# Kernel optimization log

Hardware: AMD Instinct MI355X
Metric: run time of the kernel (lower is better)

## Reference

```python
import jax, jax.numpy as jnp
import numpy as np

B, DIM_IN, DIM_OUT, K, SPK, T = 16, 256, 256, 5, 128, 8192
PAD = (K // 2, K // 2)  # odd kernel -> symmetric reflect pad


def setup_inputs() -> dict:
    key = jax.random.key(0)
    k1, k2, k3, k4 = jax.random.split(key, 4)
    x = jax.random.normal(k1, (B, DIM_IN, T), dtype=jnp.float32)
    c_trg = jax.random.normal(k2, (B, SPK), dtype=jnp.float32)
    # EqualLinear params (bias_init=1, lr_mul=1; forward uses raw weight, no scale)
    style_w = jax.random.normal(k3, (DIM_IN, SPK), dtype=jnp.float32)
    style_b = jnp.ones((DIM_IN,), dtype=jnp.float32)
    # base conv weight [1, dim_out, dim_in, k]
    weight = jax.random.normal(k4, (1, DIM_OUT, DIM_IN, K), dtype=jnp.float32)
    return {"x": x, "c_trg": c_trg, "style_w": style_w, "style_b": style_b, "weight": weight}


def _modulated_conv(x, c_trg, style_w, style_b, weight):
    # style: [B, dim_in]
    s = c_trg @ style_w.T + style_b
    # modulate: [B, dim_out, dim_in, K]
    w = weight * s[:, None, :, None]
    demod = jax.lax.rsqrt(jnp.sum(w * w, axis=(2, 3)) + 1e-8)  # [B, dim_out]
    w = w * demod[:, :, None, None]
    # reflect pad along time
    x_pad = jnp.pad(x, ((0, 0), (0, 0), PAD), mode="reflect")
    # per-sample conv1d (groups=batch in torch) via vmap
    def conv_one(xi, wi):
        # xi: [dim_in, T+K-1], wi: [dim_out, dim_in, K]
        out = jax.lax.conv_general_dilated(
            xi[None], wi, window_strides=(1,), padding="VALID",
            dimension_numbers=("NCH", "OIH", "NCH"))
        return out[0]  # [dim_out, T]
    out = jax.vmap(conv_one)(x_pad, w)
    return jax.nn.leaky_relu(out, negative_slope=0.2)


def reference(x, c_trg, style_w, style_b, weight):
    out = _modulated_conv(x, c_trg, style_w, style_b, weight)
    return (out, c_trg)
```

## Files before the change

kernel.cpp:

```cpp
#include <hip/hip_runtime.h>


#define B_    16
#define CIN   256
#define COUT  256
#define KW    5
#define SPK   128
#define TT    8192

#define OM    128
#define TN    256
#define BI    32
#define NCH   (CIN / BI)

#define XROWS 264
#define WSLAB (KW * OM * 32)
#define WMOD_BYTES ((size_t)B_ * 2 * NCH * WSLAB * 2)

typedef __attribute__((ext_vector_type(8))) short short8;
typedef __attribute__((ext_vector_type(4))) float f32x4;
typedef unsigned short ushort_t;
typedef unsigned int uint_t;

__device__ __forceinline__ ushort_t f2bf(float f) {
    uint_t u = __float_as_uint(f);
    u += 0x7FFF + ((u >> 16) & 1);
    return (ushort_t)(u >> 16);
}

__global__ __launch_bounds__(256) void prep_kernel(
    const float* __restrict__ c_trg, const float* __restrict__ style_w,
    const float* __restrict__ style_b, const float* __restrict__ weight,
    ushort_t* __restrict__ wmod)
{
    __shared__ float c_sh[SPK];
    __shared__ float s_sh[CIN];
    __shared__ float w_l[8 * 1280];
    __shared__ float dm_sh[8];

    const int og  = blockIdx.x;
    const int b   = blockIdx.y;
    const int tid = threadIdx.x;

    if (tid < SPK) c_sh[tid] = c_trg[b * SPK + tid];
    __syncthreads();
    {
        float acc = style_b[tid];
        const float* wr = style_w + (size_t)tid * SPK;
        #pragma unroll 4
        for (int j = 0; j < SPK; ++j) acc += c_sh[j] * wr[j];
        s_sh[tid] = acc;
    }
    {
        const float* wsrc = weight + (size_t)og * 8 * 1280;
        #pragma unroll
        for (int it = 0; it < 10; ++it)
            *(float4*)&w_l[(it * 256 + tid) * 4] = *(const float4*)&wsrc[(it * 256 + tid) * 4];
    }
    __syncthreads();

    {
        const int oi   = tid >> 5;
        const int part = tid & 31;
        float a = 0.f;
        #pragma unroll 8
        for (int m = 0; m < 40; ++m) {
            int j = part + m * 32;
            float v = w_l[oi * 1280 + j] * s_sh[j / 5];
            a += v * v;
        }
        a += __shfl_xor(a, 16);
        a += __shfl_xor(a, 8);
        a += __shfl_xor(a, 4);
        a += __shfl_xor(a, 2);
        a += __shfl_xor(a, 1);
        if (part == 0) dm_sh[oi] = rsqrtf(a + 1e-8f);
    }
    __syncthreads();

    for (int r = tid; r < 320; r += 256) {
        const int oi  = r / 40;
        const int rem = r - oi * 40;
        const int ch  = rem / 5;
        const int k   = rem - ch * 5;
        const int o   = og * 8 + oi;
        const int ot  = o >> 7;
        const int o_l = o & 127;
        const int swz = (o_l >> 1) & 3;
        const float dmv = dm_sh[oi];
        ushort_t* dst = wmod + ((((size_t)(b * 2 + ot) * NCH + ch) * KW + k) * OM + o_l) * 32;
        #pragma unroll
        for (int g = 0; g < 4; ++g) {
            union { ushort_t us[8]; uint4 v; } pk;
            #pragma unroll
            for (int ii = 0; ii < 8; ++ii) {
                int i_l = g * 8 + ii;
                int i_g = ch * 32 + i_l;
                pk.us[ii] = f2bf(w_l[oi * 1280 + i_g * 5 + k] * s_sh[i_g] * dmv);
            }
            *(uint4*)&dst[(g ^ swz) * 8] = pk.v;
        }
    }
}

__global__ __launch_bounds__(512, 2) void conv_mfma_ws3_kernel(
    const float* __restrict__ x, const ushort_t* __restrict__ wmod,
    float* __restrict__ out)
{
    __shared__ __align__(16) ushort_t w_sh[2][WSLAB];
    __shared__ __align__(16) ushort_t x_sh[XROWS * 32];

    const int b   = blockIdx.z;
    const int ot  = blockIdx.y;
    const int o0  = ot * OM;
    const int t0  = blockIdx.x * TN;
    const int tid = threadIdx.x;

    const int lane  = tid & 63;
    const int wv    = tid >> 6;
    const int wm    = wv >> 2;
    const int wn    = wv & 3;
    const int col16 = lane & 15;
    const int quad  = lane >> 4;

    const int rl = lane;
    const int i4 = wv;

    f32x4 acc[4][4];
    #pragma unroll
    for (int mt = 0; mt < 4; ++mt)
        #pragma unroll
        for (int nt = 0; nt < 4; ++nt)
            acc[mt][nt] = (f32x4){0.f, 0.f, 0.f, 0.f};

    const float* xb = x + (size_t)b * CIN * TT;
    const ushort_t* wslab = wmod + (size_t)(b * 2 + ot) * NCH * WSLAB;

    float xr0[20], xr1[20];

#define STAGE_W(CH, BUF) do {                                                  \
        const ushort_t* ws_ = wslab + (size_t)(CH) * WSLAB;                    \
        _Pragma("unroll")                                                      \
        for (int s_ = 0; s_ < 5; ++s_) {                                       \
            const int off_ = s_ * 4096 + wv * 512;           \
            __builtin_amdgcn_global_load_lds(                                  \
                (const __attribute__((address_space(1))) uint_t*)(ws_ + off_ + lane * 8), \
                (__attribute__((address_space(3))) uint_t*)(&w_sh[BUF][off_]), \
                16, 0, 0);                                                     \
        }                                                                      \
    } while (0)

#define LOAD_X(CH, XR) do {                                                    \
        const float* xp_ = xb + (size_t)((CH) * BI + i4 * 4) * TT;             \
        _Pragma("unroll")                                                      \
        for (int rd_ = 0; rd_ < 5; ++rd_) {                                    \
            int r_ = rd_ * 64 + rl;                                            \
            if (r_ < 260) {                                                    \
                int tg_ = t0 + r_ - 2;                                         \
                tg_ = (tg_ < 0) ? -tg_ : tg_;                                  \
                tg_ = (tg_ > TT - 1) ? (2 * (TT - 1) - tg_) : tg_;             \
                XR[rd_ * 4 + 0] = xp_[tg_];                                    \
                XR[rd_ * 4 + 1] = xp_[TT + tg_];                               \
                XR[rd_ * 4 + 2] = xp_[2 * TT + tg_];                           \
                XR[rd_ * 4 + 3] = xp_[3 * TT + tg_];                           \
            }                                                                  \
        }                                                                      \
    } while (0)

#define PUT_X(XR) do {                                                         \
        _Pragma("unroll")                                                      \
        for (int rd_ = 0; rd_ < 5; ++rd_) {                                    \
            int r_ = rd_ * 64 + rl;                                            \
            if (r_ < 260) {                                                    \
                union { ushort_t us[4]; uint2 u2; } p_;                        \
                p_.us[0] = f2bf(XR[rd_ * 4 + 0]);                              \
                p_.us[1] = f2bf(XR[rd_ * 4 + 1]);                              \
                p_.us[2] = f2bf(XR[rd_ * 4 + 2]);                              \
                p_.us[3] = f2bf(XR[rd_ * 4 + 3]);                              \
                int grp_ = (i4 >> 1) ^ ((r_ ^ (r_ >> 2)) & 3);                 \
                *(uint2*)&x_sh[r_ * 32 + grp_ * 8 + (i4 & 1) * 4] = p_.u2;     \
            }                                                                  \
        }                                                                      \
    } while (0)

#define MFMA_CHUNK(BUF) do {                                                   \
        _Pragma("unroll")                                                      \
        for (int kt_ = 0; kt_ < KW; ++kt_) {                                   \
            short8 a_[4], bf_[4];                                              \
            _Pragma("unroll")                                                  \
            for (int mt_ = 0; mt_ < 4; ++mt_) {                                \
                const int row_  = kt_ * OM + wm * 64 + mt_ * 16 + col16;       \
                const int slot_ = quad ^ ((row_ >> 1) & 3);                    \
                a_[mt_] = *(const short8*)&w_sh[BUF][row_ * 32 + slot_ * 8];   \
            }                                                                  \
            _Pragma("unroll")                                                  \
            for (int nt_ = 0; nt_ < 4; ++nt_) {                                \
                const int r_   = wn * 64 + nt_ * 16 + col16 + kt_;             \
                const int grp_ = quad ^ ((r_ ^ (r_ >> 2)) & 3);                \
                bf_[nt_] = *(const short8*)&x_sh[r_ * 32 + grp_ * 8];          \
            }                                                                  \
            _Pragma("unroll")                                                  \
            for (int mt_ = 0; mt_ < 4; ++mt_)                                  \
                _Pragma("unroll")                                              \
                for (int nt_ = 0; nt_ < 4; ++nt_)                              \
                    acc[mt_][nt_] = __builtin_amdgcn_mfma_f32_16x16x32_bf16(   \
                        a_[mt_], bf_[nt_], acc[mt_][nt_], 0, 0, 0);            \
        }                                                                      \
    } while (0)

#define CHUNK_BODY(CH, CUR, NXT, XR_CUR, XR_NXT) do {                          \
        PUT_X(XR_CUR);                                                         \
        __syncthreads();           \
        if ((CH) < NCH - 1) {                                                  \
            STAGE_W((CH) + 1, NXT);                                            \
            LOAD_X((CH) + 1, XR_NXT);                                          \
        }                                                                      \
        __builtin_amdgcn_sched_barrier(0);      \
        MFMA_CHUNK(CUR);                                                       \
        if ((CH) < NCH - 1)                                                    \
            __syncthreads();      \
                                                      \
    } while (0)

    STAGE_W(0, 0);
    LOAD_X(0, xr0);

    CHUNK_BODY(0, 0, 1, xr0, xr1);
    CHUNK_BODY(1, 1, 0, xr1, xr0);
    CHUNK_BODY(2, 0, 1, xr0, xr1);
    CHUNK_BODY(3, 1, 0, xr1, xr0);
    CHUNK_BODY(4, 0, 1, xr0, xr1);
    CHUNK_BODY(5, 1, 0, xr1, xr0);
    CHUNK_BODY(6, 0, 1, xr0, xr1);
    CHUNK_BODY(7, 1, 0, xr1, xr0);

#undef STAGE_W
#undef LOAD_X
#undef PUT_X
#undef MFMA_CHUNK
#undef CHUNK_BODY

    #pragma unroll
    for (int mt = 0; mt < 4; ++mt) {
        #pragma unroll
        for (int nt = 0; nt < 4; ++nt) {
            const int t_o = t0 + wn * 64 + nt * 16 + col16;
            #pragma unroll
            for (int reg = 0; reg < 4; ++reg) {
                const int o_l = wm * 64 + mt * 16 + quad * 4 + reg;
                float v = acc[mt][nt][reg];
                v = (v > 0.f) ? v : 0.2f * v;
                out[((size_t)(b * COUT + o0 + o_l)) * TT + t_o] = v;
            }
        }
    }
}

__global__ __launch_bounds__(256, 3) void conv_mfma_fb_kernel(
    const float* __restrict__ x, const float* __restrict__ c_trg,
    const float* __restrict__ style_w, const float* __restrict__ style_b,
    const float* __restrict__ weight, float* __restrict__ out)
{
    __shared__ ushort_t x_sh[136 * 32];
    __shared__ ushort_t w_sh[KW * 128 * 32];
    __shared__ float    c_sh[SPK];
    __shared__ float    s_sh[CIN];
    __shared__ float    dm_acc[128];
    __shared__ float    dmv[128];

    const int b   = blockIdx.z;
    const int o0  = blockIdx.y * 128;
    const int t0  = blockIdx.x * 128;
    const int tid = threadIdx.x;

    const int lane  = tid & 63;
    const int wvv   = tid >> 6;
    const int wm    = wvv >> 1;
    const int wn    = wvv & 1;
    const int col16 = lane & 15;
    const int quad  = lane >> 4;

    if (tid < SPK) c_sh[tid] = c_trg[b * SPK + tid];
    if (tid < 128) dm_acc[tid] = 0.f;
    __syncthreads();
    {
        float acc = style_b[tid];
        const float* wr = style_w + (size_t)tid * SPK;
        #pragma unroll 4
        for (int j = 0; j < SPK; ++j) acc += c_sh[j] * wr[j];
        s_sh[tid] = acc;
    }

    f32x4 acc[4][4];
    #pragma unroll
    for (int mt = 0; mt < 4; ++mt)
        #pragma unroll
        for (int nt = 0; nt < 4; ++nt)
            acc[mt][nt] = (f32x4){0.f, 0.f, 0.f, 0.f};

    const float* xb = x + (size_t)b * CIN * TT;

    for (int ch = 0; ch < NCH; ++ch) {
        const int i0 = ch * BI;
        __syncthreads();
        {
            const int i4s = tid >> 5;
            const int rls = tid & 31;
            const float* xp = xb + (size_t)(i0 + i4s * 4) * TT;
            #pragma unroll
            for (int rr = 0; rr < 136; rr += 32) {
                int r = rr + rls;
                if (r < 136) {
                    int tg = t0 + r - 2;
                    tg = (tg < 0) ? -tg : tg;
                    tg = (tg > TT - 1) ? (2 * (TT - 1) - tg) : tg;
                    float v0 = xp[tg];
                    float v1 = xp[TT + tg];
                    float v2 = xp[2 * TT + tg];
                    float v3 = xp[3 * TT + tg];
                    union { ushort_t us[4]; uint2 u2; } p;
                    p.us[0] = f2bf(v0); p.us[1] = f2bf(v1);
                    p.us[2] = f2bf(v2); p.us[3] = f2bf(v3);
                    int grp = (i4s >> 1) ^ (r & 3);
                    *(uint2*)&x_sh[r * 32 + grp * 8 + (i4s & 1) * 4] = p.u2;
                }
            }
        }
        {
            const int i4s = tid & 7;
            #pragma unroll
            for (int pass = 0; pass < 4; ++pass) {
                const int o_l = (tid >> 3) + pass * 32;
                const float* wp = weight + ((size_t)(o0 + o_l) * CIN + i0 + i4s * 4) * KW;
                float q[20];
                #pragma unroll
                for (int f = 0; f < 5; ++f)
                    *(float4*)&q[f * 4] = *(const float4*)(wp + f * 4);
                float sv0 = s_sh[i0 + i4s * 4 + 0];
                float sv1 = s_sh[i0 + i4s * 4 + 1];
                float sv2 = s_sh[i0 + i4s * 4 + 2];
                float sv3 = s_sh[i0 + i4s * 4 + 3];
                float m0[5], m1[5], m2[5], m3[5];
                float psum = 0.f;
                #pragma unroll
                for (int k = 0; k < 5; ++k) {
                    m0[k] = q[0 * 5 + k] * sv0;  psum += m0[k] * m0[k];
                    m1[k] = q[1 * 5 + k] * sv1;  psum += m1[k] * m1[k];
                    m2[k] = q[2 * 5 + k] * sv2;  psum += m2[k] * m2[k];
                    m3[k] = q[3 * 5 + k] * sv3;  psum += m3[k] * m3[k];
                }
                atomicAdd(&dm_acc[o_l], psum);
                #pragma unroll
                for (int k = 0; k < 5; ++k) {
                    union { ushort_t us[4]; uint2 u2; } p;
                    p.us[0] = f2bf(m0[k]); p.us[1] = f2bf(m1[k]);
                    p.us[2] = f2bf(m2[k]); p.us[3] = f2bf(m3[k]);
                    *(uint2*)&w_sh[(k * 128 + o_l) * 32 + i4s * 4] = p.u2;
                }
            }
        }
        __syncthreads();
        #pragma unroll
        for (int kt = 0; kt < KW; ++kt) {
            short8 a[4], bf[4];
            #pragma unroll
            for (int mt = 0; mt < 4; ++mt)
                a[mt] = *(const short8*)&w_sh[(kt * 128 + wm * 64 + mt * 16 + col16) * 32 + quad * 8];
            #pragma unroll
            for (int nt = 0; nt < 4; ++nt) {
                int r   = wn * 64 + nt * 16 + col16 + kt;
                int grp = quad ^ (r & 3);
                bf[nt] = *(const short8*)&x_sh[r * 32 + grp * 8];
            }
            #pragma unroll
            for (int mt = 0; mt < 4; ++mt)
                #pragma unroll
                for (int nt = 0; nt < 4; ++nt)
                    acc[mt][nt] = __builtin_amdgcn_mfma_f32_16x16x32_bf16(
                        a[mt], bf[nt], acc[mt][nt], 0, 0, 0);
        }
    }

    __syncthreads();
    if (tid < 128) dmv[tid] = rsqrtf(dm_acc[tid] + 1e-8f);
    __syncthreads();

    #pragma unroll
    for (int mt = 0; mt < 4; ++mt) {
        #pragma unroll
        for (int nt = 0; nt < 4; ++nt) {
            const int t_o = t0 + wn * 64 + nt * 16 + col16;
            #pragma unroll
            for (int reg = 0; reg < 4; ++reg) {
                const int o_l = wm * 64 + mt * 16 + quad * 4 + reg;
                float v = acc[mt][nt][reg] * dmv[o_l];
                v = (v > 0.f) ? v : 0.2f * v;
                out[((size_t)(b * COUT + o0 + o_l)) * TT + t_o] = v;
            }
        }
    }
}

extern "C" void kernel_launch(void* const* d_in, const int* in_sizes, int n_in,
                              void* d_out, int out_size, void* d_ws, size_t ws_size,
                              hipStream_t stream)
{
    const float* x       = (const float*)d_in[0];
    const float* c_trg   = (const float*)d_in[1];
    const float* style_w = (const float*)d_in[2];
    const float* style_b = (const float*)d_in[3];
    const float* weight  = (const float*)d_in[4];
    float* out = (float*)d_out;

    if (ws_size >= WMOD_BYTES) {
        ushort_t* wmod = (ushort_t*)d_ws;
        prep_kernel<<<dim3(32, 16), dim3(256), 0, stream>>>(
            c_trg, style_w, style_b, weight, wmod);
        conv_mfma_ws3_kernel<<<dim3(TT / TN, COUT / OM, B_), dim3(512), 0, stream>>>(
            x, wmod, out);
    } else {
        conv_mfma_fb_kernel<<<dim3(TT / 128, COUT / 128, B_), dim3(256), 0, stream>>>(
            x, c_trg, style_w, style_b, weight, out);
    }

    hipMemcpyAsync(out + (size_t)B_ * COUT * TT, c_trg,
                   (size_t)B_ * SPK * sizeof(float),
                   hipMemcpyDeviceToDevice, stream);
}
```

Before: 307.3 us.

## Apply style scale to input and demod to output instead of per-batch weights

Rather than building a modulated bf16 weight tensor for each batch sample, the prep kernel now converts the base weight to bf16 once, shared across the batch. It also computes the per-sample style vector and the demodulation factors separately. The conv kernel multiplies x by the style scale while converting it to bf16, and multiplies the accumulator by the demod factor in the epilogue. This shrinks the weight workspace by the batch factor, so the weight slabs streamed by the conv kernel are shared across samples and more likely to hit cache. The cost is a small extra multiply per x element and per output. Rounding differs slightly because the style scale is now applied to x before bf16 conversion rather than to the weights.

Result: slower. 336.6 us (+9.5%).

```diff
diff --git a/kernel.cpp b/kernel.cpp
--- a/kernel.cpp
+++ b/kernel.cpp
@@ -15,7 +15,10 @@
 
 #define XROWS 264
 #define WSLAB (KW * OM * 32)
-#define WMOD_BYTES ((size_t)B_ * 2 * NCH * WSLAB * 2)
+#define WBF_BYTES ((size_t)2 * NCH * WSLAB * 2)
+#define S_OFF   WBF_BYTES
+#define DM_OFF  (WBF_BYTES + (size_t)B_ * CIN * 4)
+#define WS_NEED (WBF_BYTES + (size_t)B_ * CIN * 4 * 2)
 
 typedef __attribute__((ext_vector_type(8))) short short8;
 typedef __attribute__((ext_vector_type(4))) float f32x4;
@@ -28,87 +31,91 @@
     return (ushort_t)(u >> 16);
 }
 
-__global__ __launch_bounds__(256) void prep_kernel(
+__global__ __launch_bounds__(256) void prep2_kernel(
     const float* __restrict__ c_trg, const float* __restrict__ style_w,
     const float* __restrict__ style_b, const float* __restrict__ weight,
-    ushort_t* __restrict__ wmod)
+    ushort_t* __restrict__ wbf, float* __restrict__ s_glob,
+    float* __restrict__ dm_glob)
 {
+    __shared__ float sm[8 * 1280];
     __shared__ float c_sh[SPK];
-    __shared__ float s_sh[CIN];
-    __shared__ float w_l[8 * 1280];
-    __shared__ float dm_sh[8];
-
-    const int og  = blockIdx.x;
-    const int b   = blockIdx.y;
+    __shared__ float s2_sh[CIN];
+
     const int tid = threadIdx.x;
 
-    if (tid < SPK) c_sh[tid] = c_trg[b * SPK + tid];
-    __syncthreads();
-    {
+    if (blockIdx.x < 32) {
+        const int og = blockIdx.x;
+        const float* wsrc = weight + (size_t)og * 8 * 1280;
+        #pragma unroll
+        for (int it = 0; it < 10; ++it)
+            *(float4*)&sm[(it * 256 + tid) * 4] = *(const float4*)&wsrc[(it * 256 + tid) * 4];
+        __syncthreads();
+
+        for (int r = tid; r < 320; r += 256) {
+            const int oi  = r / 40;
+            const int rem = r - oi * 40;
+            const int ch  = rem / 5;
+            const int k   = rem - ch * 5;
+            const int o   = og * 8 + oi;
+            const int ot  = o >> 7;
+            const int o_l = o & 127;
+            const int swz = (o_l >> 1) & 3;
+            ushort_t* dst = wbf + (((size_t)(ot * NCH + ch) * KW + k) * OM + o_l) * 32;
+            #pragma unroll
+            for (int g = 0; g < 4; ++g) {
+                union { ushort_t us[8]; uint4 v; } pk;
+                #pragma unroll
+                for (int ii = 0; ii < 8; ++ii) {
+                    int i_g = ch * 32 + g * 8 + ii;
+                    pk.us[ii] = f2bf(sm[oi * 1280 + i_g * 5 + k]);
+                }
+                *(uint4*)&dst[(g ^ swz) * 8] = pk.v;
+            }
+        }
+    } else {
+        const int b = blockIdx.x - 32;
+        if (tid < SPK) c_sh[tid] = c_trg[b * SPK + tid];
+        __syncthreads();
+
         float acc = style_b[tid];
         const float* wr = style_w + (size_t)tid * SPK;
         #pragma unroll 4
         for (int j = 0; j < SPK; ++j) acc += c_sh[j] * wr[j];
-        s_sh[tid] = acc;
-    }
-    {
-        const float* wsrc = weight + (size_t)og * 8 * 1280;
-        #pragma unroll
-        for (int it = 0; it < 10; ++it)
-            *(float4*)&w_l[(it * 256 + tid) * 4] = *(const float4*)&wsrc[(it * 256 + tid) * 4];
-    }
-    __syncthreads();
-
-    {
-        const int oi   = tid >> 5;
-        const int part = tid & 31;
+        s_glob[b * CIN + tid] = acc;
+        s2_sh[tid] = acc * acc;
+        __syncthreads();
+
+        const float* wo = weight + (size_t)tid * 1280;
         float a = 0.f;
-        #pragma unroll 8
-        for (int m = 0; m < 40; ++m) {
-            int j = part + m * 32;
-            float v = w_l[oi * 1280 + j] * s_sh[j / 5];
-            a += v * v;
-        }
-        a += __shfl_xor(a, 16);
-        a += __shfl_xor(a, 8);
-        a += __shfl_xor(a, 4);
-        a += __shfl_xor(a, 2);
-        a += __shfl_xor(a, 1);
-        if (part == 0) dm_sh[oi] = rsqrtf(a + 1e-8f);
-    }
-    __syncthreads();
-
-    for (int r = tid; r < 320; r += 256) {
-        const int oi  = r / 40;
-        const int rem = r - oi * 40;
-        const int ch  = rem / 5;
-        const int k   = rem - ch * 5;
-        const int o   = og * 8 + oi;
-        const int ot  = o >> 7;
-        const int o_l = o & 127;
-        const int swz = (o_l >> 1) & 3;
-        const float dmv = dm_sh[oi];
-        ushort_t* dst = wmod + ((((size_t)(b * 2 + ot) * NCH + ch) * KW + k) * OM + o_l) * 32;
-        #pragma unroll
-        for (int g = 0; g < 4; ++g) {
-            union { ushort_t us[8]; uint4 v; } pk;
-            #pragma unroll
-            for (int ii = 0; ii < 8; ++ii) {
-                int i_l = g * 8 + ii;
-                int i_g = ch * 32 + i_l;
-                pk.us[ii] = f2bf(w_l[oi * 1280 + i_g * 5 + k] * s_sh[i_g] * dmv);
-            }
-            *(uint4*)&dst[(g ^ swz) * 8] = pk.v;
-        }
+        #pragma unroll 4
+        for (int ig = 0; ig < 64; ++ig) {
+            float q[20];
+            #pragma unroll
+            for (int f = 0; f < 5; ++f)
+                *(float4*)&q[f * 4] = *(const float4*)&wo[ig * 20 + f * 4];
+            #pragma unroll
+            for (int c = 0; c < 4; ++c) {
+                const float s2 = s2_sh[ig * 4 + c];
+                #pragma unroll
+                for (int k = 0; k < 5; ++k) {
+                    const float v = q[c * 5 + k];
+                    a += v * v * s2;
+                }
+            }
+        }
+        dm_glob[b * COUT + tid] = rsqrtf(a + 1e-8f);
     }
 }
 
-__global__ __launch_bounds__(512, 2) void conv_mfma_ws3_kernel(
-    const float* __restrict__ x, const ushort_t* __restrict__ wmod,
+__global__ __launch_bounds__(512, 2) void conv_mfma_ws4_kernel(
+    const float* __restrict__ x, const ushort_t* __restrict__ wbf,
+    const float* __restrict__ s_glob, const float* __restrict__ dm_glob,
     float* __restrict__ out)
 {
     __shared__ __align__(16) ushort_t w_sh[2][WSLAB];
     __shared__ __align__(16) ushort_t x_sh[XROWS * 32];
+    __shared__ float s_lds[CIN];
+    __shared__ float dm_lds[OM];
 
     const int b   = blockIdx.z;
     const int ot  = blockIdx.y;
@@ -134,7 +141,7 @@
             acc[mt][nt] = (f32x4){0.f, 0.f, 0.f, 0.f};
 
     const float* xb = x + (size_t)b * CIN * TT;
-    const ushort_t* wslab = wmod + (size_t)(b * 2 + ot) * NCH * WSLAB;
+    const ushort_t* wslab = wbf + (size_t)ot * NCH * WSLAB;
 
     float xr0[20], xr1[20];
 
@@ -167,16 +174,20 @@
         }                                                                      \
     } while (0)
 
-#define PUT_X(XR) do {                                                         \
+#define PUT_X(CH, XR) do {                                                     \
+        const float s0_ = s_lds[(CH) * BI + i4 * 4 + 0];                       \
+        const float s1_ = s_lds[(CH) * BI + i4 * 4 + 1];                       \
+        const float s2_ = s_lds[(CH) * BI + i4 * 4 + 2];                       \
+        const float s3_ = s_lds[(CH) * BI + i4 * 4 + 3];                       \
         _Pragma("unroll")                                                      \
         for (int rd_ = 0; rd_ < 5; ++rd_) {                                    \
             int r_ = rd_ * 64 + rl;                                            \
             if (r_ < 260) {                                                    \
                 union { ushort_t us[4]; uint2 u2; } p_;                        \
-                p_.us[0] = f2bf(XR[rd_ * 4 + 0]);                              \
-                p_.us[1] = f2bf(XR[rd_ * 4 + 1]);                              \
-                p_.us[2] = f2bf(XR[rd_ * 4 + 2]);                              \
-                p_.us[3] = f2bf(XR[rd_ * 4 + 3]);                              \
+                p_.us[0] = f2bf(XR[rd_ * 4 + 0] * s0_);                        \
+                p_.us[1] = f2bf(XR[rd_ * 4 + 1] * s1_);                        \
+                p_.us[2] = f2bf(XR[rd_ * 4 + 2] * s2_);                        \
+                p_.us[3] = f2bf(XR[rd_ * 4 + 3] * s3_);                        \
                 int grp_ = (i4 >> 1) ^ ((r_ ^ (r_ >> 2)) & 3);                 \
                 *(uint2*)&x_sh[r_ * 32 + grp_ * 8 + (i4 & 1) * 4] = p_.u2;     \
             }                                                                  \
@@ -209,21 +220,23 @@
     } while (0)
 
 #define CHUNK_BODY(CH, CUR, NXT, XR_CUR, XR_NXT) do {                          \
-        PUT_X(XR_CUR);                                                         \
-        __syncthreads();           \
+        PUT_X(CH, XR_CUR);                                                     \
+        __syncthreads();                                                       \
         if ((CH) < NCH - 1) {                                                  \
             STAGE_W((CH) + 1, NXT);                                            \
             LOAD_X((CH) + 1, XR_NXT);                                          \
         }                                                                      \
-        __builtin_amdgcn_sched_barrier(0);      \
+        __builtin_amdgcn_sched_barrier(0);                                     \
         MFMA_CHUNK(CUR);                                                       \
         if ((CH) < NCH - 1)                                                    \
-            __syncthreads();      \
-                                                      \
+            __syncthreads();                                                   \
     } while (0)
 
+    if (tid < CIN) s_lds[tid] = s_glob[b * CIN + tid];
+    if (tid < OM)  dm_lds[tid] = dm_glob[b * COUT + o0 + tid];
     STAGE_W(0, 0);
     LOAD_X(0, xr0);
+    __syncthreads();
 
     CHUNK_BODY(0, 0, 1, xr0, xr1);
     CHUNK_BODY(1, 1, 0, xr1, xr0);
@@ -248,7 +261,7 @@
             #pragma unroll
             for (int reg = 0; reg < 4; ++reg) {
                 const int o_l = wm * 64 + mt * 16 + quad * 4 + reg;
-                float v = acc[mt][nt][reg];
+                float v = acc[mt][nt][reg] * dm_lds[o_l];
                 v = (v > 0.f) ? v : 0.2f * v;
                 out[((size_t)(b * COUT + o0 + o_l)) * TT + t_o] = v;
             }
@@ -412,12 +425,14 @@
     const float* weight  = (const float*)d_in[4];
     float* out = (float*)d_out;
 
-    if (ws_size >= WMOD_BYTES) {
-        ushort_t* wmod = (ushort_t*)d_ws;
-        prep_kernel<<<dim3(32, 16), dim3(256), 0, stream>>>(
-            c_trg, style_w, style_b, weight, wmod);
-        conv_mfma_ws3_kernel<<<dim3(TT / TN, COUT / OM, B_), dim3(512), 0, stream>>>(
-            x, wmod, out);
+    if (ws_size >= WS_NEED) {
+        ushort_t* wbf   = (ushort_t*)d_ws;
+        float* s_glob   = (float*)((char*)d_ws + S_OFF);
+        float* dm_glob  = (float*)((char*)d_ws + DM_OFF);
+        prep2_kernel<<<dim3(48), dim3(256), 0, stream>>>(
+            c_trg, style_w, style_b, weight, wbf, s_glob, dm_glob);
+        conv_mfma_ws4_kernel<<<dim3(TT / TN, COUT / OM, B_), dim3(512), 0, stream>>>(
+            x, wbf, s_glob, dm_glob, out);
     } else {
         conv_mfma_fb_kernel<<<dim3(TT / 128, COUT / 128, B_), dim3(256), 0, stream>>>(
             x, c_trg, style_w, style_b, weight, out);
```
